# Kernel tuning notes

Hardware: AMD Instinct MI355X
Metric: run time of the kernel (lower is better)

## Reference

```python
import jax, jax.numpy as jnp
import numpy as np

DIM = 4096
N_HEADS = 32
HEAD_DIM = DIM // N_HEADS  # 128
BSZ = 2
SEQLEN = 2048


def setup_inputs() -> dict:
    key = jax.random.key(0)
    ks = jax.random.split(key, 8)
    x = jax.random.normal(ks[0], (BSZ, SEQLEN, DIM), dtype=jnp.float32)
    # rotary frequencies (LLaMA): theta = 10000^{-2i/d}, angle = pos * theta
    inv_freq = 1.0 / (10000.0 ** (np.arange(0, HEAD_DIM, 2, dtype=np.float32) / HEAD_DIM))
    angles = np.arange(SEQLEN, dtype=np.float32)[:, None] * inv_freq[None, :]  # [S, hd/2]
    freqs_cos = jnp.asarray(np.cos(angles))
    freqs_sin = jnp.asarray(np.sin(angles))
    # causal additive mask [1,1,S,S]
    neg = jnp.float32(-1e9)
    mask = jnp.where(jnp.tril(jnp.ones((SEQLEN, SEQLEN), dtype=bool)), 0.0, neg)[None, None]
    scale = 0.02
    wq = jax.random.normal(ks[1], (DIM, DIM), dtype=jnp.float32) * scale
    wk = jax.random.normal(ks[2], (DIM, DIM), dtype=jnp.float32) * scale
    wv = jax.random.normal(ks[3], (DIM, DIM), dtype=jnp.float32) * scale
    wo = jax.random.normal(ks[4], (DIM, DIM), dtype=jnp.float32) * scale
    return {"x": x, "start_pos": 0, "freqs_cos": freqs_cos, "freqs_sin": freqs_sin,
            "mask": mask, "wq": wq, "wk": wk, "wv": wv, "wo": wo}


def _apply_rotary(t, cos, sin):
    # t: [B,S,H,hd]; cos/sin: [S,hd/2] -> broadcast [1,S,1,hd/2]
    t = t.reshape(*t.shape[:-1], HEAD_DIM // 2, 2)
    t0, t1 = t[..., 0], t[..., 1]
    c = cos[None, :, None, :]
    s = sin[None, :, None, :]
    r0 = t0 * c - t1 * s
    r1 = t0 * s + t1 * c
    return jnp.stack([r0, r1], axis=-1).reshape(*t0.shape[:-1], HEAD_DIM)


def reference(x, start_pos, freqs_cos, freqs_sin, mask, wq, wk, wv, wo):
    bsz, seqlen, _ = x.shape
    # QKV projections (nn.Linear: y = x @ W.T; weights stored [out,in])
    xq = (x @ wq.T).reshape(bsz, seqlen, N_HEADS, HEAD_DIM)
    xk = (x @ wk.T).reshape(bsz, seqlen, N_HEADS, HEAD_DIM)
    xv = (x @ wv.T).reshape(bsz, seqlen, N_HEADS, HEAD_DIM)
    xq = _apply_rotary(xq, freqs_cos, freqs_sin)
    xk = _apply_rotary(xk, freqs_cos, freqs_sin)
    # [B,H,S,hd]
    q = xq.transpose(0, 2, 1, 3)
    k = xk.transpose(0, 2, 1, 3)
    v = xv.transpose(0, 2, 1, 3)
    scale = 1.0 / jnp.sqrt(jnp.float32(HEAD_DIM))
    scores = jnp.einsum('bhqd,bhkd->bhqk', q, k) * scale + mask
    probs = jax.nn.softmax(scores, axis=-1)
    out = jnp.einsum('bhqk,bhkd->bhqd', probs, v)  # [B,H,S,hd]
    out = out.transpose(0, 2, 1, 3).reshape(bsz, seqlen, DIM)
    return out @ wo.T
```

## Files before the change

kernel.cpp:

```cpp
#include <hip/hip_runtime.h>

typedef unsigned short ushort_t;
typedef unsigned int u32;
typedef short bf16x8 __attribute__((ext_vector_type(8)));
typedef float f32x4 __attribute__((ext_vector_type(4)));
typedef float f32x16 __attribute__((ext_vector_type(16)));
typedef u32 u32x4 __attribute__((ext_vector_type(4)));

__device__ __forceinline__ ushort_t f2bf(float f) {
  u32 u = __builtin_bit_cast(u32, f);
  u += 0x7FFFu + ((u >> 16) & 1u);
  return (ushort_t)(u >> 16);
}
__device__ __forceinline__ float bf2f(u32 bits16) {
  return __builtin_bit_cast(float, bits16 << 16);
}

__device__ __forceinline__ void cvt_body(const float* __restrict__ in,
                                         ushort_t* __restrict__ out, int i) {
  const float4 a = ((const float4*)in)[(size_t)i * 2];
  const float4 b = ((const float4*)in)[(size_t)i * 2 + 1];
  uint4 r;
  r.x = (u32)f2bf(a.x) | ((u32)f2bf(a.y) << 16);
  r.y = (u32)f2bf(a.z) | ((u32)f2bf(a.w) << 16);
  r.z = (u32)f2bf(b.x) | ((u32)f2bf(b.y) << 16);
  r.w = (u32)f2bf(b.z) | ((u32)f2bf(b.w) << 16);
  ((uint4*)out)[i] = r;
}

__device__ __forceinline__ void cvt_perm_body(const float* __restrict__ in,
                                              ushort_t* __restrict__ out, int i) {
  const int row = i >> 9, k8 = i & 511;
  const int q = row & 31;
  const int lrow = (row & ~31) | ((q < 16) ? (2 * q) : (2 * (q - 16) + 1));
  const float4 a = ((const float4*)in)[(size_t)lrow * 1024 + k8 * 2];
  const float4 b = ((const float4*)in)[(size_t)lrow * 1024 + k8 * 2 + 1];
  uint4 r;
  r.x = (u32)f2bf(a.x) | ((u32)f2bf(a.y) << 16);
  r.y = (u32)f2bf(a.z) | ((u32)f2bf(a.w) << 16);
  r.z = (u32)f2bf(b.x) | ((u32)f2bf(b.y) << 16);
  r.w = (u32)f2bf(b.z) | ((u32)f2bf(b.w) << 16);
  ((uint4*)out)[(size_t)row * 512 + k8] = r;
}

__global__ __launch_bounds__(256)
void cvt2_kernel(const float* __restrict__ i0, ushort_t* __restrict__ o0,
                 const float* __restrict__ i1, ushort_t* __restrict__ o1,
                 const float* __restrict__ fcos, const float* __restrict__ fsin,
                 float2* __restrict__ cst) {
  const int i = blockIdx.x * 256 + threadIdx.x;
  if (blockIdx.y == 0) {
    if (blockIdx.x < 512) cst[i] = make_float2(fcos[i], fsin[i]);
    cvt_body(i0, o0, i);
  } else {
    cvt_perm_body(i1, o1, i);
  }
}

template <int F32OUT, int ROPE, int CVT>
__global__ __launch_bounds__(512, 2)
void gemm256(const ushort_t* __restrict__ A, const ushort_t* __restrict__ B,
             void* __restrict__ C, const float2* __restrict__ cst, float qsc,
             const float* __restrict__ csrc, ushort_t* __restrict__ cdst) {
  constexpr int KD = 4096, ND = 4096;
  __shared__ ushort_t sA[2][2][128 * 64];
  __shared__ ushort_t sB[2][2][128 * 64];
  const int tid = threadIdx.x;
  const int id = blockIdx.x;
  if (CVT && id >= 256) {
    const int cb_ = id - 256;
#pragma unroll 2
    for (int it = 0; it < 8; ++it) {
      const int i = it * 262144 + cb_ * 512 + tid;
      if (CVT == 1) cvt_perm_body(csrc, cdst, i);
      else cvt_body(csrc, cdst, i);
    }
    return;
  }
  const int lane = tid & 63, wave = tid >> 6;
  const int lq = lane & 15, g = lane >> 4;
  const int wm = wave >> 2, wn = wave & 3;
  const int swz = (id & 7) * 32 + (id >> 3);
  const int bm = (swz >> 4) * 256;
  const int bn = (swz & 15) * 256;
  const int csw = ((lane & 7) ^ (lane >> 3)) * 8;
  const int srow = lane >> 3;

  f32x4 acc[8][4];
#pragma unroll
  for (int m = 0; m < 8; ++m)
#pragma unroll
    for (int n = 0; n < 4; ++n) acc[m][n] = (f32x4)0.f;

#define STG(sbuf, G, rowb, t_, s_, h_)                                               \
  {                                                                                  \
    _Pragma("unroll") for (int i_ = 0; i_ < 2; ++i_) {                               \
      const int r0_ = wave * 16 + i_ * 8;                                            \
      const int tc_ = (t_) > 63 ? 63 : (t_);                                         \
      const ushort_t* src_ =                                                         \
          (G) + (size_t)((rowb) + (h_) * 128 + r0_ + srow) * KD + tc_ * 64 + csw;    \
      __builtin_amdgcn_global_load_lds(                                              \
          (const __attribute__((address_space(1))) u32*)src_,                        \
          (__attribute__((address_space(3))) u32*)&sbuf[s_][h_][r0_ * 64 + lane * 8],\
          16, 0, 0);                                                                 \
    }                                                                                \
  }
#define RD_A(S_, H_, mf_, kk_)                                                        \
  (*(const bf16x8*)&sA[S_][H_][(wm * 64 + (mf_) * 16 + lq) * 64 +                     \
                               ((((kk_) * 4 + g) ^ (lq & 7)) * 8)])
#define RD_B(S_, H_, nf_, kk_)                                                        \
  (*(const bf16x8*)&sB[S_][H_][(wn * 32 + (nf_) * 16 + lq) * 64 +                     \
                               ((((kk_) * 4 + g) ^ (lq & 7)) * 8)])
#define MM2(MB, B0R, B1R)                                                             \
  _Pragma("unroll") for (int mf = 0; mf < 4; ++mf)                                    \
    _Pragma("unroll") for (int nf = 0; nf < 2; ++nf)                                  \
      _Pragma("unroll") for (int kk = 0; kk < 2; ++kk) {                              \
        acc[(MB) + mf][nf] = __builtin_amdgcn_mfma_f32_16x16x32_bf16(                 \
            af[mf][kk], B0R[nf][kk], acc[(MB) + mf][nf], 0, 0, 0);                    \
        acc[(MB) + mf][2 + nf] = __builtin_amdgcn_mfma_f32_16x16x32_bf16(             \
            af[mf][kk], B1R[nf][kk], acc[(MB) + mf][2 + nf], 0, 0, 0);                \
      }

  STG(sA, A, bm, 0, 0, 0); STG(sA, A, bm, 0, 0, 1);
  STG(sB, B, bn, 0, 0, 0); STG(sB, B, bn, 0, 0, 1);
  asm volatile("s_waitcnt vmcnt(0)" ::: "memory");
  __builtin_amdgcn_s_barrier();
  __builtin_amdgcn_sched_barrier(0);

  bf16x8 af[4][2], b0[2][2], b1[2][2];

#define TILE(S_, T_)                                                                  \
  STG(sA, A, bm, (T_) + 1, (S_) ^ 1, 0);                                              \
  STG(sA, A, bm, (T_) + 1, (S_) ^ 1, 1);                                              \
  STG(sB, B, bn, (T_) + 1, (S_) ^ 1, 0);                                              \
  STG(sB, B, bn, (T_) + 1, (S_) ^ 1, 1);                                              \
  _Pragma("unroll") for (int mf = 0; mf < 4; ++mf)                                    \
    _Pragma("unroll") for (int kk = 0; kk < 2; ++kk)                                  \
      af[mf][kk] = RD_A(S_, 0, mf, kk);                                               \
  _Pragma("unroll") for (int nf = 0; nf < 2; ++nf)                                    \
    _Pragma("unroll") for (int kk = 0; kk < 2; ++kk) {                                \
      b0[nf][kk] = RD_B(S_, 0, nf, kk);                                               \
      b1[nf][kk] = RD_B(S_, 1, nf, kk);                                               \
    }                                                                                 \
  __builtin_amdgcn_s_setprio(1);                                                      \
  MM2(0, b0, b1);                                                                     \
  __builtin_amdgcn_s_setprio(0);                                                      \
  _Pragma("unroll") for (int mf = 0; mf < 4; ++mf)                                    \
    _Pragma("unroll") for (int kk = 0; kk < 2; ++kk)                                  \
      af[mf][kk] = RD_A(S_, 1, mf, kk);                                               \
  __builtin_amdgcn_s_setprio(1);                                                      \
  MM2(4, b0, b1);                                                                     \
  __builtin_amdgcn_s_setprio(0);                                                      \
  asm volatile("s_waitcnt vmcnt(0)" ::: "memory");                                    \
  __builtin_amdgcn_s_barrier();                                                       \
  __builtin_amdgcn_sched_barrier(0);

  for (int t = 0; t < 64; t += 2) {
    TILE(0, t)
    TILE(1, t + 1)
  }
#undef TILE
#undef STG
#undef RD_A
#undef RD_B
#undef MM2

  if (ROPE) {
    const int p = wn * 16 + lq;
#pragma unroll
    for (int m = 0; m < 8; ++m) {
      const int grow = bm + (m >> 2) * 128 + wm * 64 + (m & 3) * 16 + g * 4;
#pragma unroll
      for (int r = 0; r < 4; ++r) {
        const int row = grow + r;
        const float2 cs = cst[(size_t)(row & 2047) * 64 + p];
#pragma unroll
        for (int pr = 0; pr < 2; ++pr) {
          const float t0 = acc[m][pr * 2][r];
          const float t1 = acc[m][pr * 2 + 1][r];
          const int c0 = bn + pr * 128 + wn * 32 + lq;
          ((ushort_t*)C)[(size_t)row * ND + c0] =
              f2bf((t0 * cs.x - t1 * cs.y) * qsc);
          ((ushort_t*)C)[(size_t)row * ND + c0 + 16] =
              f2bf((t0 * cs.y + t1 * cs.x) * qsc);
        }
      }
    }
  } else {
#pragma unroll
    for (int m = 0; m < 8; ++m) {
      const int grow = bm + (m >> 2) * 128 + wm * 64 + (m & 3) * 16 + g * 4;
#pragma unroll
      for (int r = 0; r < 4; ++r) {
        const int row = grow + r;
#pragma unroll
        for (int n = 0; n < 4; ++n) {
          const int gcol = bn + (n >> 1) * 128 + wn * 32 + (n & 1) * 16 + lq;
          if (F32OUT)
            ((float*)C)[(size_t)row * ND + gcol] = acc[m][n][r];
          else
            ((ushort_t*)C)[(size_t)row * ND + gcol] = f2bf(acc[m][n][r]);
        }
      }
    }
  }
}

__global__ __launch_bounds__(256, 2)
void attn_kernel(const ushort_t* __restrict__ Q, const ushort_t* __restrict__ K,
                 const ushort_t* __restrict__ Vt, ushort_t* __restrict__ O,
                 const float* __restrict__ csrc, ushort_t* __restrict__ cdst) {
  __shared__ ushort_t sK[2][32 * 128];
  __shared__ ushort_t sV[2][128 * 32];
  __shared__ float sScr[4][32];

  const int bp = blockIdx.x;
  if (bp >= 512) {
    const int cb_ = bp - 512;
#pragma unroll 2
    for (int it = 0; it < 16; ++it)
      cvt_body(csrc, cdst, it * 131072 + cb_ * 256 + threadIdx.x);
    return;
  }

  const int lane = threadIdx.x & 63, wave = threadIdx.x >> 6;
  const int lq = lane & 31, hi = lane >> 5;
  const int bh = bp >> 3, j = bp & 7;
  const int h = bh & 31, b = bh >> 5;
  const ushort_t* Kb_ = K + (size_t)(b * 2048) * 4096 + h * 128;
  const ushort_t* Vb_ = Vt + (size_t)(h * 128) * 4096 + b * 2048;

#define STAGE(buf, kt_)                                                              \
  {                                                                                  \
    const int kb_ = (kt_) * 32;                                                      \
    _Pragma("unroll")                                                                \
    for (int i_ = 0; i_ < 2; ++i_) {                                                 \
      const int c_ = wave + i_ * 4;                                                  \
      const int krow = c_ * 4 + (lane >> 4);                                         \
      const int kcol = (lane & 15) ^ (krow & 7);                                     \
      const ushort_t* ksrc = Kb_ + (size_t)(kb_ + krow) * 4096 + kcol * 8;           \
      __builtin_amdgcn_global_load_lds(                                              \
          (const __attribute__((address_space(1))) u32*)ksrc,                        \
          (__attribute__((address_space(3))) u32*)&sK[buf][c_ * 512 + lane * 8],     \
          16, 0, 0);                                                                 \
      const int sst = c_ * 64 + lane;                                                \
      const int dv = sst >> 2;                                                       \
      const int gl = (sst & 3) ^ ((sst >> 3) & 3);                                   \
      const ushort_t* vsrc = Vb_ + (size_t)dv * 4096 + kb_ + gl * 8;                 \
      __builtin_amdgcn_global_load_lds(                                              \
          (const __attribute__((address_space(1))) u32*)vsrc,                        \
          (__attribute__((address_space(3))) u32*)&sV[buf][sst * 8], 16, 0, 0);      \
    }                                                                                \
  }

  for (int ph = 0; ph < 2; ++ph) {
    const int qj = ph ? (15 - j) : j;
    const int qbase = qj * 128 + wave * 32;
    const int ntw = qj * 4 + wave + 1;
    const int ntmax = qj * 4 + 4;

    bf16x8 aq[8];
    const ushort_t* qrow = Q + (size_t)(b * 2048 + qbase + lq) * 4096 + h * 128 + hi * 8;
#pragma unroll
    for (int kf = 0; kf < 8; ++kf) aq[kf] = *(const bf16x8*)(qrow + kf * 16);

    f32x16 o[4];
#pragma unroll
    for (int dt = 0; dt < 4; ++dt) o[dt] = (f32x16)0.f;
    float m_run = -1e30f, l_run = 0.f;

    int cur = 0;
    STAGE(0, 0);
    __syncthreads();

    for (int kt = 0; kt < ntmax; ++kt) {
      if (kt + 1 < ntmax) STAGE(cur ^ 1, kt + 1);
      if (kt < ntw) {
        const int kb = kt * 32;
        f32x16 st = (f32x16)0.f;
#pragma unroll
        for (int kf = 0; kf < 8; ++kf) {
          const bf16x8 kfrag =
              *(const bf16x8*)&sK[cur][lq * 128 + (((kf * 2 + hi) ^ (lq & 7)) * 8)];
          st = __builtin_amdgcn_mfma_f32_32x32x16_bf16(kfrag, aq[kf], st, 0, 0, 0);
        }
        if (kt == ntw - 1) {
          const int q = qbase + lq;
#pragma unroll
          for (int r = 0; r < 16; ++r) {
            const int key = kb + (r & 3) + 8 * (r >> 2) + 4 * hi;
            if (key > q) st[r] = -1e30f;
          }
        }
        float tm = st[0];
#pragma unroll
        for (int r = 1; r < 16; ++r) tm = fmaxf(tm, st[r]);
        tm = fmaxf(tm, __shfl_xor(tm, 32));
        if (!__all(tm <= m_run + 8.f)) {
          const float mnew = fmaxf(m_run, tm);
          const float corr = __expf(m_run - mnew);
          m_run = mnew;
          l_run *= corr;
          if (hi == 0) sScr[wave][lq] = corr;
          float fr[16];
#pragma unroll
          for (int r = 0; r < 16; ++r)
            fr[r] = sScr[wave][(r & 3) + 8 * (r >> 2) + 4 * hi];
#pragma unroll
          for (int dt = 0; dt < 4; ++dt)
#pragma unroll
            for (int r = 0; r < 16; ++r) o[dt][r] *= fr[r];
        }
        float rs = 0.f;
#pragma unroll
        for (int r = 0; r < 16; ++r) { st[r] = __expf(st[r] - m_run); rs += st[r]; }
        rs += __shfl_xor(rs, 32);
        l_run += rs;
        u32 A_, B_, C_, D_, E_, F_, G_, H_;
#define CVTPK(d_, l_, h_) \
  asm("v_cvt_pk_bf16_f32 %0, %1, %2" : "=v"(d_) : "v"(l_), "v"(h_))
        CVTPK(A_, st[0], st[1]);  CVTPK(B_, st[4], st[5]);
        CVTPK(C_, st[2], st[3]);  CVTPK(D_, st[6], st[7]);
        CVTPK(E_, st[8], st[9]);  CVTPK(F_, st[12], st[13]);
        CVTPK(G_, st[10], st[11]); CVTPK(H_, st[14], st[15]);
#undef CVTPK
        asm volatile("v_permlane32_swap_b32 %0, %1" : "+v"(A_), "+v"(B_));
        asm volatile("v_permlane32_swap_b32 %0, %1" : "+v"(C_), "+v"(D_));
        asm volatile("v_permlane32_swap_b32 %0, %1" : "+v"(E_), "+v"(F_));
        asm volatile("v_permlane32_swap_b32 %0, %1" : "+v"(G_), "+v"(H_));
        const bf16x8 pa0 = __builtin_bit_cast(bf16x8, (u32x4){A_, C_, B_, D_});
        const bf16x8 pa1 = __builtin_bit_cast(bf16x8, (u32x4){E_, G_, F_, H_});
#pragma unroll
        for (int dt = 0; dt < 4; ++dt) {
          const int d0 = dt * 32 + lq;
          const int s0 = 4 * d0 + ((hi + 0) ^ ((d0 >> 1) & 3));
          const int s1 = 4 * d0 + ((hi + 2) ^ ((d0 >> 1) & 3));
          const bf16x8 vf0 = *(const bf16x8*)&sV[cur][s0 * 8];
          const bf16x8 vf1 = *(const bf16x8*)&sV[cur][s1 * 8];
          o[dt] = __builtin_amdgcn_mfma_f32_32x32x16_bf16(pa0, vf0, o[dt], 0, 0, 0);
          o[dt] = __builtin_amdgcn_mfma_f32_32x32x16_bf16(pa1, vf1, o[dt], 0, 0, 0);
        }
      }
      __syncthreads();
      cur ^= 1;
    }

    if (hi == 0) sScr[wave][lq] = 1.f / l_run;
    __syncthreads();
    const size_t obase = (size_t)(b * 2048 + qbase) * 4096 + h * 128;
#pragma unroll
    for (int r = 0; r < 16; ++r) {
      const int qr = (r & 3) + 8 * (r >> 2) + 4 * hi;
      const float f = sScr[wave][qr];
#pragma unroll
      for (int dt = 0; dt < 4; ++dt)
        O[obase + (size_t)qr * 4096 + dt * 32 + lq] = f2bf(o[dt][r] * f);
    }
    __syncthreads();
  }
#undef STAGE
}

extern "C" void kernel_launch(void* const* d_in, const int* in_sizes, int n_in,
                              void* d_out, int out_size, void* d_ws, size_t ws_size,
                              hipStream_t stream) {
  const float* x = (const float*)d_in[0];
  const float* fcos = (const float*)d_in[2];
  const float* fsin = (const float*)d_in[3];
  const float* wq = (const float*)d_in[5];
  const float* wk = (const float*)d_in[6];
  const float* wv = (const float*)d_in[7];
  const float* wo = (const float*)d_in[8];
  float* out = (float*)d_out;
  char* ws = (char*)d_ws;
  const size_t MB32 = 33554432;
  ushort_t* xb = (ushort_t*)(ws);
  ushort_t* wb = (ushort_t*)(ws + MB32);
  ushort_t* Qb = (ushort_t*)(ws + 2 * MB32);
  ushort_t* Kb = (ushort_t*)(ws + 3 * MB32);
  ushort_t* Vt = (ushort_t*)(ws + 4 * MB32);
  ushort_t* Ob = xb;
  float2* cst = (float2*)d_out;

  const dim3 cb(256);
  const dim3 gb(512);
  const float QSC = 0.08838834764831845f;

  hipLaunchKernelGGL(cvt2_kernel, dim3(8192, 2), cb, 0, stream, x, xb, wq, wb,
                     fcos, fsin, cst);
  hipLaunchKernelGGL((gemm256<0, 1, 1>), dim3(768), gb, 0, stream, xb, wb,
                     (void*)Qb, cst, QSC, wk, Vt);
  hipLaunchKernelGGL((gemm256<0, 1, 2>), dim3(768), gb, 0, stream, xb, Vt,
                     (void*)Kb, cst, 1.f, wv, wb);
  hipLaunchKernelGGL((gemm256<0, 0, 0>), dim3(256), gb, 0, stream, wb, xb,
                     (void*)Vt, cst, 1.f, nullptr, nullptr);
  hipLaunchKernelGGL(attn_kernel, dim3(1024), cb, 0, stream, Qb, Kb, Vt, Ob, wo, wb);
  hipLaunchKernelGGL((gemm256<1, 0, 0>), dim3(256), gb, 0, stream, Ob, wb,
                     (void*)out, cst, 1.f, nullptr, nullptr);
}
```

Baseline: 657.8 us.

## Switch GEMM to triple-buffered K=32 stages with contiguous 256-row tiles

The GEMM mainloop now uses a three-stage LDS ring of 256x32 K-slices instead of double-buffered 256x64 slices split into halves. Loads are issued two tiles ahead, and the wait drops to vmcnt(4) so one prefetch stays in flight across the barrier. The wave-to-tile mapping also changes to contiguous 128x64 subtiles per wave with a new XOR swizzle, and the RoPE and store epilogues are remapped to match. This is meant to hide global-load latency better, at the cost of twice as many barriers per K and less MFMA work between them.

```diff
diff --git a/kernel.cpp b/kernel.cpp
--- a/kernel.cpp
+++ b/kernel.cpp
@@ -63,8 +63,8 @@
              void* __restrict__ C, const float2* __restrict__ cst, float qsc,
              const float* __restrict__ csrc, ushort_t* __restrict__ cdst) {
   constexpr int KD = 4096, ND = 4096;
-  __shared__ ushort_t sA[2][2][128 * 64];
-  __shared__ ushort_t sB[2][2][128 * 64];
+  __shared__ ushort_t sA[3][256 * 32];
+  __shared__ ushort_t sB[3][256 * 32];
   const int tid = threadIdx.x;
   const int id = blockIdx.x;
   if (CVT && id >= 256) {
@@ -83,8 +83,7 @@
   const int swz = (id & 7) * 32 + (id >> 3);
   const int bm = (swz >> 4) * 256;
   const int bn = (swz & 15) * 256;
-  const int csw = ((lane & 7) ^ (lane >> 3)) * 8;
-  const int srow = lane >> 3;
+  const int rsw = (g ^ ((lq >> 1) & 3)) * 8;
 
   f32x4 acc[8][4];
 #pragma unroll
@@ -92,93 +91,73 @@
 #pragma unroll
     for (int n = 0; n < 4; ++n) acc[m][n] = (f32x4)0.f;
 
-#define STG(sbuf, G, rowb, t_, s_, h_)                                               \
+#define STG(sbuf, G, rowb, t_, s_)                                                   \
   {                                                                                  \
     _Pragma("unroll") for (int i_ = 0; i_ < 2; ++i_) {                               \
-      const int r0_ = wave * 16 + i_ * 8;                                            \
-      const int tc_ = (t_) > 63 ? 63 : (t_);                                         \
-      const ushort_t* src_ =                                                         \
-          (G) + (size_t)((rowb) + (h_) * 128 + r0_ + srow) * KD + tc_ * 64 + csw;    \
+      const int j_ = i_ * 512 + wave * 64 + lane;                                    \
+      const int r_ = j_ >> 2, cp_ = j_ & 3;                                          \
+      const int tc_ = (t_) > 127 ? 127 : (t_);                                       \
+      const ushort_t* src_ = (G) + (size_t)((rowb) + r_) * KD + tc_ * 32 +           \
+                             ((cp_ ^ ((r_ >> 1) & 3)) * 8);                          \
       __builtin_amdgcn_global_load_lds(                                              \
           (const __attribute__((address_space(1))) u32*)src_,                        \
-          (__attribute__((address_space(3))) u32*)&sbuf[s_][h_][r0_ * 64 + lane * 8],\
-          16, 0, 0);                                                                 \
+          (__attribute__((address_space(3))) u32*)&sbuf[s_][j_ * 8], 16, 0, 0);      \
     }                                                                                \
   }
-#define RD_A(S_, H_, mf_, kk_)                                                        \
-  (*(const bf16x8*)&sA[S_][H_][(wm * 64 + (mf_) * 16 + lq) * 64 +                     \
-                               ((((kk_) * 4 + g) ^ (lq & 7)) * 8)])
-#define RD_B(S_, H_, nf_, kk_)                                                        \
-  (*(const bf16x8*)&sB[S_][H_][(wn * 32 + (nf_) * 16 + lq) * 64 +                     \
-                               ((((kk_) * 4 + g) ^ (lq & 7)) * 8)])
-#define MM2(MB, B0R, B1R)                                                             \
-  _Pragma("unroll") for (int mf = 0; mf < 4; ++mf)                                    \
-    _Pragma("unroll") for (int nf = 0; nf < 2; ++nf)                                  \
-      _Pragma("unroll") for (int kk = 0; kk < 2; ++kk) {                              \
-        acc[(MB) + mf][nf] = __builtin_amdgcn_mfma_f32_16x16x32_bf16(                 \
-            af[mf][kk], B0R[nf][kk], acc[(MB) + mf][nf], 0, 0, 0);                    \
-        acc[(MB) + mf][2 + nf] = __builtin_amdgcn_mfma_f32_16x16x32_bf16(             \
-            af[mf][kk], B1R[nf][kk], acc[(MB) + mf][2 + nf], 0, 0, 0);                \
-      }
-
-  STG(sA, A, bm, 0, 0, 0); STG(sA, A, bm, 0, 0, 1);
-  STG(sB, B, bn, 0, 0, 0); STG(sB, B, bn, 0, 0, 1);
-  asm volatile("s_waitcnt vmcnt(0)" ::: "memory");
+#define RD_A(S_, mf_)                                                                 \
+  (*(const bf16x8*)&sA[S_][(wm * 128 + (mf_) * 16 + lq) * 32 + rsw])
+#define RD_B(S_, nf_)                                                                 \
+  (*(const bf16x8*)&sB[S_][(wn * 64 + (nf_) * 16 + lq) * 32 + rsw])
+
+  STG(sA, A, bm, 0, 0); STG(sB, B, bn, 0, 0);
+  STG(sA, A, bm, 1, 1); STG(sB, B, bn, 1, 1);
+  asm volatile("s_waitcnt vmcnt(4)" ::: "memory");
   __builtin_amdgcn_s_barrier();
   __builtin_amdgcn_sched_barrier(0);
 
-  bf16x8 af[4][2], b0[2][2], b1[2][2];
-
-#define TILE(S_, T_)                                                                  \
-  STG(sA, A, bm, (T_) + 1, (S_) ^ 1, 0);                                              \
-  STG(sA, A, bm, (T_) + 1, (S_) ^ 1, 1);                                              \
-  STG(sB, B, bn, (T_) + 1, (S_) ^ 1, 0);                                              \
-  STG(sB, B, bn, (T_) + 1, (S_) ^ 1, 1);                                              \
-  _Pragma("unroll") for (int mf = 0; mf < 4; ++mf)                                    \
-    _Pragma("unroll") for (int kk = 0; kk < 2; ++kk)                                  \
-      af[mf][kk] = RD_A(S_, 0, mf, kk);                                               \
-  _Pragma("unroll") for (int nf = 0; nf < 2; ++nf)                                    \
-    _Pragma("unroll") for (int kk = 0; kk < 2; ++kk) {                                \
-      b0[nf][kk] = RD_B(S_, 0, nf, kk);                                               \
-      b1[nf][kk] = RD_B(S_, 1, nf, kk);                                               \
-    }                                                                                 \
+  bf16x8 af[8], bfr[4];
+
+#define TILE(S_, S2_, T_)                                                             \
+  STG(sA, A, bm, (T_) + 2, S2_);                                                      \
+  STG(sB, B, bn, (T_) + 2, S2_);                                                      \
+  _Pragma("unroll") for (int mf = 0; mf < 8; ++mf) af[mf] = RD_A(S_, mf);             \
+  _Pragma("unroll") for (int nf = 0; nf < 4; ++nf) bfr[nf] = RD_B(S_, nf);            \
   __builtin_amdgcn_s_setprio(1);                                                      \
-  MM2(0, b0, b1);                                                                     \
+  _Pragma("unroll") for (int mf = 0; mf < 8; ++mf)                                    \
+    _Pragma("unroll") for (int nf = 0; nf < 4; ++nf)                                  \
+      acc[mf][nf] = __builtin_amdgcn_mfma_f32_16x16x32_bf16(af[mf], bfr[nf],          \
+                                                            acc[mf][nf], 0, 0, 0);   \
   __builtin_amdgcn_s_setprio(0);                                                      \
-  _Pragma("unroll") for (int mf = 0; mf < 4; ++mf)                                    \
-    _Pragma("unroll") for (int kk = 0; kk < 2; ++kk)                                  \
-      af[mf][kk] = RD_A(S_, 1, mf, kk);                                               \
-  __builtin_amdgcn_s_setprio(1);                                                      \
-  MM2(4, b0, b1);                                                                     \
-  __builtin_amdgcn_s_setprio(0);                                                      \
-  asm volatile("s_waitcnt vmcnt(0)" ::: "memory");                                    \
+  asm volatile("s_waitcnt vmcnt(4)" ::: "memory");                                    \
   __builtin_amdgcn_s_barrier();                                                       \
   __builtin_amdgcn_sched_barrier(0);
 
-  for (int t = 0; t < 64; t += 2) {
-    TILE(0, t)
-    TILE(1, t + 1)
-  }
+  for (int t = 0; t < 126; t += 3) {
+    TILE(0, 2, t)
+    TILE(1, 0, t + 1)
+    TILE(2, 1, t + 2)
+  }
+  TILE(0, 2, 126)
+  TILE(1, 0, 127)
 #undef TILE
 #undef STG
 #undef RD_A
 #undef RD_B
-#undef MM2
 
   if (ROPE) {
-    const int p = wn * 16 + lq;
-#pragma unroll
-    for (int m = 0; m < 8; ++m) {
-      const int grow = bm + (m >> 2) * 128 + wm * 64 + (m & 3) * 16 + g * 4;
+#pragma unroll
+    for (int mf = 0; mf < 8; ++mf) {
+      const int grow = bm + wm * 128 + mf * 16 + g * 4;
 #pragma unroll
       for (int r = 0; r < 4; ++r) {
         const int row = grow + r;
-        const float2 cs = cst[(size_t)(row & 2047) * 64 + p];
 #pragma unroll
         for (int pr = 0; pr < 2; ++pr) {
-          const float t0 = acc[m][pr * 2][r];
-          const float t1 = acc[m][pr * 2 + 1][r];
-          const int c0 = bn + pr * 128 + wn * 32 + lq;
+          const int p = ((wn * 2 + pr) & 3) * 16 + lq;
+          const float2 cs = cst[(size_t)(row & 2047) * 64 + p];
+          const float t0 = acc[mf][pr * 2][r];
+          const float t1 = acc[mf][pr * 2 + 1][r];
+          const int c0 = bn + wn * 64 + pr * 32 + lq;
           ((ushort_t*)C)[(size_t)row * ND + c0] =
               f2bf((t0 * cs.x - t1 * cs.y) * qsc);
           ((ushort_t*)C)[(size_t)row * ND + c0 + 16] =
@@ -188,18 +167,18 @@
     }
   } else {
 #pragma unroll
-    for (int m = 0; m < 8; ++m) {
-      const int grow = bm + (m >> 2) * 128 + wm * 64 + (m & 3) * 16 + g * 4;
+    for (int mf = 0; mf < 8; ++mf) {
+      const int grow = bm + wm * 128 + mf * 16 + g * 4;
 #pragma unroll
       for (int r = 0; r < 4; ++r) {
         const int row = grow + r;
 #pragma unroll
-        for (int n = 0; n < 4; ++n) {
-          const int gcol = bn + (n >> 1) * 128 + wn * 32 + (n & 1) * 16 + lq;
+        for (int nf = 0; nf < 4; ++nf) {
+          const int gcol = bn + wn * 64 + nf * 16 + lq;
           if (F32OUT)
-            ((float*)C)[(size_t)row * ND + gcol] = acc[m][n][r];
+            ((float*)C)[(size_t)row * ND + gcol] = acc[mf][nf][r];
           else
-            ((ushort_t*)C)[(size_t)row * ND + gcol] = f2bf(acc[m][n][r]);
+            ((ushort_t*)C)[(size_t)row * ND + gcol] = f2bf(acc[mf][nf][r]);
         }
       }
     }
```

Measured after the change: 739.6 us. +12.4%, slower.
